# Performance work log

Hardware: AMD Instinct MI355X
Metric: run time of the kernel (lower is better)

The kernel has to match this reference:

```python
import jax, jax.numpy as jnp
from jax import lax
import numpy as np

# dims
N_DIA, DLEN = 48, 64            # 48 dialogues, 64 utterances each
N = N_DIA * DLEN                # total utterances = 3072
D = 512                         # n_dim (modal feature dim)
H = 512                         # nhidden
NL = 2                          # GCNII layers
NS = 2                          # n_speakers
ALPHA, LAMDA = 0.1, 0.5
PI = float(np.pi)
SCALE = 0.99999                 # acos clamp factor from original code


def setup_inputs() -> dict:
    key = jax.random.key(0)
    ks = jax.random.split(key, 8)
    a = jax.random.normal(ks[0], (N, D), jnp.float32)
    v = jax.random.normal(ks[1], (N, D), jnp.float32)
    l = jax.random.normal(ks[2], (N, D), jnp.float32)
    qmask = jax.random.uniform(ks[3], (DLEN, N_DIA, NS), jnp.float32)
    dia_len = np.full((N_DIA,), DLEN, dtype=np.int64)  # static segment lengths
    # learned params
    W_spk = 0.02 * jax.random.normal(ks[4], (NS, D), jnp.float32)      # speaker_embeddings
    W0 = jax.random.normal(ks[5], (D, H), jnp.float32) / np.sqrt(D)    # graph_net.fcs[0]
    b0 = jnp.zeros((H,), jnp.float32)
    Wg = jax.random.normal(ks[6], (NL, H, H), jnp.float32) / np.sqrt(H)  # GCNII conv weights
    return {"a": a, "v": v, "l": l, "qmask": qmask, "dia_len": dia_len,
            "W_spk": W_spk, "W0": W0, "b0": b0, "Wg": Wg}


def _angular_sim(cs):
    # 1 - acos(cs*0.99999)/pi, clipped for numerical safety of acos
    return 1.0 - jnp.arccos(jnp.clip(cs * SCALE, -SCALE, SCALE)) / PI


def _build_adj(feats, seg_mask):
    # feats: list of 3 arrays [N, D]; seg_mask: [N, N] same-dialogue block mask
    n = feats[0].shape[0]
    normed = [f * jax.lax.rsqrt(jnp.sum(f * f, axis=1, keepdims=True)) for f in feats]
    adj = jnp.zeros((3 * n, 3 * n), feats[0].dtype)
    ar = jnp.arange(n)
    for m in range(3):
        for nn_ in range(3):
            if m == nn_:
                # within-modality: block-diagonal (per dialogue) angular cosine similarity
                sim = _angular_sim(normed[m] @ normed[m].T) * seg_mask
                adj = adj.at[m * n:(m + 1) * n, nn_ * n:(nn_ + 1) * n].set(sim)
            else:
                # cross-modality: only diagonal (same utterance) entries
                cs = jnp.sum(normed[m] * normed[nn_], axis=1)
                adj = adj.at[m * n + ar, nn_ * n + ar].set(_angular_sim(cs))
    # symmetric degree normalization D^-1/2 A D^-1/2
    dinv = jax.lax.rsqrt(adj.sum(axis=1))
    return adj * dinv[:, None] * dinv[None, :]


def reference(a, v, l, qmask, dia_len, W_spk, W0, b0, Wg):
    dl = np.asarray(dia_len)
    nb = dl.shape[0]
    # node -> (position-in-dialogue, dialogue-id), static from dia_len
    dia_id = np.repeat(np.arange(nb), dl)
    pos = np.concatenate([np.arange(x) for x in dl])
    qflat = qmask[pos, dia_id]                 # [N, NS], matches torch.cat order
    spk_idx = jnp.argmax(qflat, axis=-1)       # [N]
    l = l + W_spk[spk_idx]                     # use_speaker=True, 'l' in modals

    seg = jnp.asarray(dia_id)
    seg_mask = (seg[:, None] == seg[None, :]).astype(a.dtype)  # [N, N]
    adj = _build_adj([a, v, l], seg_mask)      # [3N, 3N]

    x = jnp.concatenate([a, v, l], axis=0)     # [3N, D]
    # GCNII_lyc (eval mode: dropout is identity)
    h0 = jax.nn.relu(x @ W0 + b0)              # [3N, H]
    thetas = jnp.log(LAMDA / jnp.arange(1, NL + 1, dtype=x.dtype) + 1.0)

    def step(h, wt):
        W, theta = wt
        hi = adj @ h
        support = (1.0 - ALPHA) * hi + ALPHA * h0   # variant=False
        h = jax.nn.relu(theta * (support @ W) + (1.0 - theta) * support)
        return h, None

    h, _ = lax.scan(step, h0, (Wg, thetas))
    feat = jnp.concatenate([x, h], axis=-1)    # use_residue=True -> [3N, D+H]
    n = a.shape[0]
    # regroup per-utterance modal features: [N, 3*(D+H)]
    out = jnp.concatenate([feat[:n], feat[n:2 * n], feat[2 * n:3 * n]], axis=-1)
    return out
```

## Files before the change

### kernel.cpp

```cpp
#include <hip/hip_runtime.h>
#include <math.h>

#define N_DIA 48
#define NTOT  3072
#define DD    512
#define M3    9216
#define SEG   ((size_t)NTOT * DD)

#define SCALE_F 0.99999f
#define PI_F    3.14159274101257324f

typedef __attribute__((ext_vector_type(8))) short frag8;
typedef __attribute__((ext_vector_type(4))) float f32x4;

__device__ __forceinline__ float ang_sim(float cs) {
    float cc = cs * SCALE_F;
    cc = fminf(fmaxf(cc, -SCALE_F), SCALE_F);
    return 1.0f - acosf(cc) / PI_F;
}
__device__ __forceinline__ unsigned short f2bf(float x) {
    union { float f; unsigned int u; } c; c.f = x;
    unsigned int r = c.u + 0x7fffu + ((c.u >> 16) & 1u);
    return (unsigned short)(r >> 16);
}
__device__ __forceinline__ float bf2f(unsigned short h) {
    union { unsigned int u; float f; } c; c.u = ((unsigned int)h) << 16;
    return c.f;
}
__device__ __forceinline__ void gload16(const unsigned short* g, unsigned short* s) {
    __builtin_amdgcn_global_load_lds(
        (const __attribute__((address_space(1))) unsigned int*)g,
        (__attribute__((address_space(3))) unsigned int*)s, 16, 0, 0);
}

__global__ __launch_bounds__(256) void k_pre_wt(
    const float* __restrict__ a, const float* __restrict__ v,
    const float* __restrict__ l, const float* __restrict__ qmask,
    const float* __restrict__ Wspk, const float* __restrict__ W0,
    const float* __restrict__ Wg,
    float* __restrict__ out, unsigned short* __restrict__ xb,
    float* __restrict__ invn, float* __restrict__ cross,
    unsigned short* __restrict__ Wt)
{
    __shared__ float tile[32][33];
    int b = blockIdx.x;
    if (b < 768) {
        int wv = threadIdx.x >> 6, t = threadIdx.x & 63;
        int i = b * 4 + wv;
        int pos = i & 63, dia = i >> 6;
        int qb = (pos * N_DIA + dia) * 2;
        float q0 = qmask[qb], q1 = qmask[qb + 1];
        int spk = (q0 >= q1) ? 0 : 1;
        const float4* av4 = (const float4*)(a + (size_t)i * DD);
        const float4* vv4 = (const float4*)(v + (size_t)i * DD);
        const float4* lv4 = (const float4*)(l + (size_t)i * DD);
        const float4* wv4 = (const float4*)(Wspk + (size_t)spk * DD);
        float* ob = out + (size_t)i * 3072;
        float saa = 0, svv = 0, sll = 0, sav = 0, sal = 0, svl = 0;
#pragma unroll
        for (int e = 0; e < 2; e++) {
            int idx = e * 64 + t;
            float4 xa = av4[idx], xv = vv4[idx], xd = lv4[idx], xw = wv4[idx];
            float4 xL = make_float4(xd.x + xw.x, xd.y + xw.y, xd.z + xw.z, xd.w + xw.w);
            *(float4*)(ob + idx * 4)        = xa;
            *(float4*)(ob + 1024 + idx * 4) = xv;
            *(float4*)(ob + 2048 + idx * 4) = xL;
            ushort4 ya, yv, yl;
            ya.x = f2bf(xa.x); ya.y = f2bf(xa.y); ya.z = f2bf(xa.z); ya.w = f2bf(xa.w);
            yv.x = f2bf(xv.x); yv.y = f2bf(xv.y); yv.z = f2bf(xv.z); yv.w = f2bf(xv.w);
            yl.x = f2bf(xL.x); yl.y = f2bf(xL.y); yl.z = f2bf(xL.z); yl.w = f2bf(xL.w);
            *(ushort4*)(xb + (size_t)i * DD + idx * 4) = ya;
            *(ushort4*)(xb + SEG + (size_t)i * DD + idx * 4) = yv;
            *(ushort4*)(xb + 2 * SEG + (size_t)i * DD + idx * 4) = yl;
            saa += xa.x * xa.x + xa.y * xa.y + xa.z * xa.z + xa.w * xa.w;
            svv += xv.x * xv.x + xv.y * xv.y + xv.z * xv.z + xv.w * xv.w;
            sll += xL.x * xL.x + xL.y * xL.y + xL.z * xL.z + xL.w * xL.w;
            sav += xa.x * xv.x + xa.y * xv.y + xa.z * xv.z + xa.w * xv.w;
            sal += xa.x * xL.x + xa.y * xL.y + xa.z * xL.z + xa.w * xL.w;
            svl += xv.x * xL.x + xv.y * xL.y + xv.z * xL.z + xv.w * xL.w;
        }
#pragma unroll
        for (int off = 32; off; off >>= 1) {
            saa += __shfl_down(saa, off, 64);
            svv += __shfl_down(svv, off, 64);
            sll += __shfl_down(sll, off, 64);
            sav += __shfl_down(sav, off, 64);
            sal += __shfl_down(sal, off, 64);
            svl += __shfl_down(svl, off, 64);
        }
        if (t == 0) {
            float ina = 1.0f / sqrtf(saa);
            float inv_ = 1.0f / sqrtf(svv);
            float inl = 1.0f / sqrtf(sll);
            invn[i] = ina; invn[NTOT + i] = inv_; invn[2 * NTOT + i] = inl;
            cross[i]            = ang_sim(sav * ina * inv_);
            cross[NTOT + i]     = ang_sim(sal * ina * inl);
            cross[2 * NTOT + i] = ang_sim(svl * inv_ * inl);
        }
    } else {
        int idx = b - 768;
        int mm = idx >> 8;
        int by = (idx >> 4) & 15, bx = idx & 15;
        const float* W = (mm == 0) ? W0 : Wg + (size_t)(mm - 1) * DD * DD;
        int t = threadIdx.x, tx = t & 31, ty = t >> 5;
#pragma unroll
        for (int q = 0; q < 4; q++) {
            int k = by * 32 + ty + q * 8;
            tile[ty + q * 8][tx] = W[(size_t)k * DD + bx * 32 + tx];
        }
        __syncthreads();
#pragma unroll
        for (int q = 0; q < 4; q++) {
            int n = bx * 32 + ty + q * 8;
            Wt[(size_t)mm * DD * DD + (size_t)n * DD + by * 32 + tx] = f2bf(tile[tx][ty + q * 8]);
        }
    }
}

__global__ __launch_bounds__(256) void k_g0_gram(
    const unsigned short* __restrict__ xb, const unsigned short* __restrict__ Wt,
    const float* __restrict__ bias, unsigned short* __restrict__ h0,
    const float* __restrict__ invn, const float* __restrict__ cross,
    float* __restrict__ blk, float* __restrict__ dinv)
{
    __shared__ __align__(16) char smem[53248];
    int b = blockIdx.x;
    int t = threadIdx.x, lane = t & 63, wv = t >> 6;
    int rsel = lane & 15, quad = lane >> 4;

    if (b < 144) {
        unsigned short* Xs = (unsigned short*)smem;
        int d = b % N_DIA, m = b / N_DIA;
        int mrow = m * NTOT + d * 64;
        const unsigned short* src = xb + (size_t)mrow * DD;
        int sunit = ((t & 3) ^ ((t >> 2) & 3)) * 8;
        int sq = (quad ^ (rsel & 3)) * 8;
        f32x4 acc[4];
#pragma unroll
        for (int j = 0; j < 4; j++) acc[j] = (f32x4){0.f, 0.f, 0.f, 0.f};
#pragma unroll
        for (int p = 0; p < 2; p++) {
            if (p) __syncthreads();
#pragma unroll
            for (int c = 0; c < 8; c++) {
                gload16(src + (size_t)(t >> 2) * DD + (p * 8 + c) * 32 + sunit,
                        &Xs[c * 2048 + wv * 512]);
            }
            __syncthreads();
#pragma unroll
            for (int c = 0; c < 8; c++) {
                const unsigned short* base = &Xs[c * 2048];
                frag8 bf[4];
#pragma unroll
                for (int j = 0; j < 4; j++)
                    bf[j] = *(const frag8*)&base[(j * 16 + rsel) * 32 + sq];
                frag8 af = *(const frag8*)&base[(wv * 16 + rsel) * 32 + sq];
#pragma unroll
                for (int j = 0; j < 4; j++)
                    acc[j] = __builtin_amdgcn_mfma_f32_16x16x32_bf16(af, bf[j], acc[j], 0, 0, 0);
            }
        }

        size_t bbase = (size_t)(m * N_DIA + d) * 4096;
        int rowl0 = wv * 16 + quad * 4;
        float ir[4], rs[4] = {0.f, 0.f, 0.f, 0.f};
#pragma unroll
        for (int r = 0; r < 4; r++) ir[r] = invn[mrow + rowl0 + r];
#pragma unroll
        for (int j = 0; j < 4; j++) {
            int coll = j * 16 + rsel;
            float ic = invn[mrow + coll];
#pragma unroll
            for (int r = 0; r < 4; r++) {
                float sim = ang_sim(acc[j][r] * ir[r] * ic);
                blk[bbase + (size_t)(rowl0 + r) * 64 + coll] = sim;
                rs[r] += sim;
            }
        }
#pragma unroll
        for (int off = 8; off; off >>= 1)
#pragma unroll
            for (int r = 0; r < 4; r++) rs[r] += __shfl_down(rs[r], off, 16);
        if (rsel == 0) {
#pragma unroll
            for (int r = 0; r < 4; r++) {
                int gi = d * 64 + rowl0 + r;
                float c1, c2;
                if (m == 0)      { c1 = cross[gi];        c2 = cross[NTOT + gi]; }
                else if (m == 1) { c1 = cross[gi];        c2 = cross[2 * NTOT + gi]; }
                else             { c1 = cross[NTOT + gi]; c2 = cross[2 * NTOT + gi]; }
                dinv[m * NTOT + gi] = 1.0f / sqrtf(rs[r] + c1 + c2);
            }
        }
        return;
    }

    unsigned short* const As0 = (unsigned short*)smem;
    unsigned short* const As1 = (unsigned short*)(smem + 8192);
    unsigned short* const Bs0 = (unsigned short*)(smem + 16384);
    unsigned short* const Bs1 = (unsigned short*)(smem + 32768);
    unsigned short* const tR  = (unsigned short*)(smem + 17408);

    int b2 = b - 144;
    int bx = b2 & 3, by = b2 >> 2;
    int mbase = by * 64, nbase = bx * 128;
    int r8 = lane >> 3, u8 = lane & 7;
    int su8 = (u8 ^ r8) << 3;

    const unsigned short* Ag = xb + (size_t)(mbase + wv * 8 + r8) * DD + su8;
    const unsigned short* Bg = Wt + (size_t)(nbase + wv * 8 + r8) * DD + su8;

    f32x4 acc[8];
#pragma unroll
    for (int i = 0; i < 8; i++) acc[i] = (f32x4){0.f, 0.f, 0.f, 0.f};

#define STAGE64(kt, Asb, Bsb) do { \
    gload16(Ag + (kt) * 64,                    (Asb) + (wv * 8) * 64); \
    gload16(Ag + (size_t)32 * DD + (kt) * 64,  (Asb) + (32 + wv * 8) * 64); \
    gload16(Bg + (kt) * 64,                    (Bsb) + (wv * 8) * 64); \
    gload16(Bg + (size_t)32 * DD + (kt) * 64,  (Bsb) + (32 + wv * 8) * 64); \
    gload16(Bg + (size_t)64 * DD + (kt) * 64,  (Bsb) + (64 + wv * 8) * 64); \
    gload16(Bg + (size_t)96 * DD + (kt) * 64,  (Bsb) + (96 + wv * 8) * 64); \
} while (0)

    STAGE64(0, As0, Bs0);
#pragma unroll
    for (int kt = 0; kt < 8; kt++) {
        __syncthreads();
        const unsigned short* Ac = (kt & 1) ? As1 : As0;
        const unsigned short* Bc = (kt & 1) ? Bs1 : Bs0;
        if (kt < 7) {
            unsigned short* An = (kt & 1) ? As0 : As1;
            unsigned short* Bn = (kt & 1) ? Bs0 : Bs1;
            STAGE64(kt + 1, An, Bn);
        }
#pragma unroll
        for (int ks = 0; ks < 2; ks++) {
            int su = (((ks << 2) + quad) ^ (rsel & 7)) << 3;
            frag8 af[4], bfr[2];
#pragma unroll
            for (int i = 0; i < 4; i++)
                af[i] = *(const frag8*)&Ac[(i * 16 + rsel) * 64 + su];
#pragma unroll
            for (int j = 0; j < 2; j++)
                bfr[j] = *(const frag8*)&Bc[(wv * 32 + j * 16 + rsel) * 64 + su];
#pragma unroll
            for (int i = 0; i < 4; i++)
#pragma unroll
                for (int j = 0; j < 2; j++)
                    acc[i * 2 + j] = __builtin_amdgcn_mfma_f32_16x16x32_bf16(
                        af[i], bfr[j], acc[i * 2 + j], 0, 0, 0);
        }
    }
#undef STAGE64
    __syncthreads();

#pragma unroll
    for (int i = 0; i < 4; i++)
#pragma unroll
        for (int j = 0; j < 2; j++) {
            int cl = wv * 32 + j * 16 + rsel;
            float bv = bias[nbase + cl];
#pragma unroll
            for (int rr = 0; rr < 4; rr++) {
                float x = fmaxf(acc[i * 2 + j][rr] + bv, 0.f);
                tR[(i * 16 + quad * 4 + rr) * 136 + cl] = f2bf(x);
            }
        }
    __syncthreads();
    {
        int r = t >> 2, c0 = (t & 3) * 32;
        unsigned short* dst = h0 + (size_t)(mbase + r) * DD + nbase + c0;
#pragma unroll
        for (int u = 0; u < 4; u++)
            *(uint4*)(dst + u * 8) = *(const uint4*)&tR[r * 136 + c0 + u * 8];
    }
}

__global__ __launch_bounds__(256) void k_gemm(
    const unsigned short* __restrict__ A, const unsigned short* __restrict__ W,
    unsigned short* __restrict__ oRows, unsigned short* __restrict__ oT,
    float theta,
    const unsigned short* __restrict__ A2, unsigned short* __restrict__ oRows2)
{
    __shared__ __align__(16) char smem[53248];
    unsigned short* const As0 = (unsigned short*)smem;
    unsigned short* const As1 = (unsigned short*)(smem + 8192);
    unsigned short* const Bs0 = (unsigned short*)(smem + 16384);
    unsigned short* const Bs1 = (unsigned short*)(smem + 32768);
    unsigned short* const tH  = (unsigned short*)smem;
    unsigned short* const tR  = (unsigned short*)(smem + 17408);
    unsigned short* const tT  = (unsigned short*)(smem + 34816);

    int t = threadIdx.x, lane = t & 63, wv = t >> 6;
    int bx = blockIdx.x, by = blockIdx.y;
    const unsigned short* Ap = A;
    unsigned short* oR = oRows;
    unsigned short* oTp = oT;
    if (by >= 144) { Ap = A2; oR = oRows2; oTp = nullptr; by -= 144; }
    int mbase = by * 64, nbase = bx * 128;
    int rsel = lane & 15, quad = lane >> 4;
    int r8 = lane >> 3, u8 = lane & 7;
    int su8 = (u8 ^ r8) << 3;

    const unsigned short* Ag = Ap + (size_t)(mbase + wv * 8 + r8) * DD + su8;
    const unsigned short* Bg = W  + (size_t)(nbase + wv * 8 + r8) * DD + su8;

    f32x4 acc[8];
#pragma unroll
    for (int i = 0; i < 8; i++) acc[i] = (f32x4){0.f, 0.f, 0.f, 0.f};

#define STAGE64(kt, Asb, Bsb) do { \
    gload16(Ag + (kt) * 64,                    (Asb) + (wv * 8) * 64); \
    gload16(Ag + (size_t)32 * DD + (kt) * 64,  (Asb) + (32 + wv * 8) * 64); \
    gload16(Bg + (kt) * 64,                    (Bsb) + (wv * 8) * 64); \
    gload16(Bg + (size_t)32 * DD + (kt) * 64,  (Bsb) + (32 + wv * 8) * 64); \
    gload16(Bg + (size_t)64 * DD + (kt) * 64,  (Bsb) + (64 + wv * 8) * 64); \
    gload16(Bg + (size_t)96 * DD + (kt) * 64,  (Bsb) + (96 + wv * 8) * 64); \
} while (0)

    STAGE64(0, As0, Bs0);
#pragma unroll
    for (int kt = 0; kt < 8; kt++) {
        __syncthreads();
        const unsigned short* Ac = (kt & 1) ? As1 : As0;
        const unsigned short* Bc = (kt & 1) ? Bs1 : Bs0;
        if (kt < 7) {
            unsigned short* An = (kt & 1) ? As0 : As1;
            unsigned short* Bn = (kt & 1) ? Bs0 : Bs1;
            STAGE64(kt + 1, An, Bn);
        }
#pragma unroll
        for (int ks = 0; ks < 2; ks++) {
            int su = (((ks << 2) + quad) ^ (rsel & 7)) << 3;
            frag8 af[4], bfr[2];
#pragma unroll
            for (int i = 0; i < 4; i++)
                af[i] = *(const frag8*)&Ac[(i * 16 + rsel) * 64 + su];
#pragma unroll
            for (int j = 0; j < 2; j++)
                bfr[j] = *(const frag8*)&Bc[(wv * 32 + j * 16 + rsel) * 64 + su];
#pragma unroll
            for (int i = 0; i < 4; i++)
#pragma unroll
                for (int j = 0; j < 2; j++)
                    acc[i * 2 + j] = __builtin_amdgcn_mfma_f32_16x16x32_bf16(
                        af[i], bfr[j], acc[i * 2 + j], 0, 0, 0);
        }
    }
#undef STAGE64
    __syncthreads();

    int r = t >> 2, c0 = (t & 3) * 32;
    {
        const unsigned short* srcA = Ap + (size_t)(mbase + r) * DD + nbase + c0;
#pragma unroll
        for (int u = 0; u < 4; u++)
            *(uint4*)&tH[r * 136 + c0 + u * 8] = *(const uint4*)(srcA + u * 8);
        __syncthreads();
    }
    float omt = 1.0f - theta;
#pragma unroll
    for (int i = 0; i < 4; i++)
#pragma unroll
        for (int j = 0; j < 2; j++) {
            int cl = wv * 32 + j * 16 + rsel;
            float vv[4];
#pragma unroll
            for (int rr = 0; rr < 4; rr++) {
                int rl = i * 16 + quad * 4 + rr;
                vv[rr] = theta * acc[i * 2 + j][rr] + omt * bf2f(tH[rl * 136 + cl]);
            }
#pragma unroll
            for (int rr = 0; rr < 4; rr++)
                tR[(i * 16 + quad * 4 + rr) * 136 + cl] = f2bf(vv[rr]);
            if (oTp) {
                ushort4 w4;
                w4.x = f2bf(vv[0]); w4.y = f2bf(vv[1]);
                w4.z = f2bf(vv[2]); w4.w = f2bf(vv[3]);
                *(ushort4*)&tT[cl * 72 + i * 16 + quad * 4] = w4;
            }
        }
    __syncthreads();
    {
        unsigned short* dst = oR + (size_t)(mbase + r) * DD + nbase + c0;
#pragma unroll
        for (int u = 0; u < 4; u++)
            *(uint4*)(dst + u * 8) = *(const uint4*)&tR[r * 136 + c0 + u * 8];
    }
    if (oTp) {
        int c = t >> 1, r0 = (t & 1) * 32;
        unsigned short* dst = oTp + (size_t)(nbase + c) * M3 + mbase + r0;
#pragma unroll
        for (int u = 0; u < 4; u++)
            *(uint4*)(dst + u * 8) = *(const uint4*)&tT[c * 72 + r0 + u * 8];
    }
}

__global__ __launch_bounds__(256) void k_adj(
    const float* __restrict__ blk, const float* __restrict__ cross,
    const float* __restrict__ dinv,
    const unsigned short* __restrict__ GT, const unsigned short* __restrict__ Gr,
    const unsigned short* __restrict__ P0,
    unsigned short* __restrict__ hout, float* __restrict__ outF, int final_mode)
{
    __shared__ __align__(16) unsigned short AdL[64 * 64];
    __shared__ __align__(16) unsigned short GTL[128 * 64];
    __shared__ __align__(16) unsigned short OT[64 * 136];
    __shared__ float dv[64];
    int ch = blockIdx.x, d = blockIdx.y, m = blockIdx.z;
    int t = threadIdx.x;
    int lane = t & 63, wv = t >> 6;
    int dbase = d * 64, cbase = ch * 128;
    int rsel = lane & 15, quad = lane >> 4;

    if (t < 64) dv[t] = dinv[m * NTOT + dbase + t];
    __syncthreads();

    size_t bbase = (size_t)(m * N_DIA + d) * 4096;
#pragma unroll
    for (int q = 0; q < 4; q++) {
        int e4 = t + 256 * q;
        int i = e4 >> 4, j4 = e4 & 15;
        float4 w = *(const float4*)(blk + bbase + (size_t)i * 64 + j4 * 4);
        float di = dv[i];
        ushort4 o;
        o.x = f2bf(w.x * di * dv[j4 * 4 + 0]);
        o.y = f2bf(w.y * di * dv[j4 * 4 + 1]);
        o.z = f2bf(w.z * di * dv[j4 * 4 + 2]);
        o.w = f2bf(w.w * di * dv[j4 * 4 + 3]);
        *(ushort4*)((char*)AdL + i * 128 + (((j4 >> 1) ^ (i & 7)) << 4) + ((j4 & 1) << 3)) = o;
    }
#pragma unroll
    for (int p = 0; p < 4; p++) {
        int e = t + 256 * p;
        int cl = e >> 3;
        int uo = e & 7;
        uint4 w = *(const uint4*)(GT + (size_t)(cbase + cl) * M3 + m * NTOT + dbase + uo * 8);
        *(uint4*)((char*)GTL + cl * 128 + ((uo ^ (cl & 7)) << 4)) = w;
    }
    __syncthreads();

    f32x4 acc[8];
#pragma unroll
    for (int i = 0; i < 8; i++) acc[i] = (f32x4){0.f, 0.f, 0.f, 0.f};
#pragma unroll
    for (int kk = 0; kk < 2; kk++) {
        int su = ((kk * 4 + quad) ^ (rsel & 7)) << 4;
        frag8 bfr[4];
#pragma unroll
        for (int it = 0; it < 4; it++)
            bfr[it] = *(const frag8*)((const char*)AdL + (it * 16 + rsel) * 128 + su);
#pragma unroll
        for (int jc = 0; jc < 2; jc++) {
            frag8 af = *(const frag8*)((const char*)GTL + (wv * 32 + jc * 16 + rsel) * 128 + su);
#pragma unroll
            for (int it = 0; it < 4; it++)
                acc[jc * 4 + it] = __builtin_amdgcn_mfma_f32_16x16x32_bf16(
                    af, bfr[it], acc[jc * 4 + it], 0, 0, 0);
        }
    }

    int n1, n2, p1, p2;
    if (m == 0)      { n1 = 1; n2 = 2; p1 = 0; p2 = 1; }
    else if (m == 1) { n1 = 0; n2 = 2; p1 = 0; p2 = 2; }
    else             { n1 = 0; n2 = 1; p1 = 1; p2 = 2; }
#pragma unroll
    for (int it = 0; it < 4; it++) {
        int il = it * 16 + rsel;
        int gi = dbase + il;
        float dm = dv[il];
        float cv1 = cross[p1 * NTOT + gi] * dm * dinv[n1 * NTOT + gi];
        float cv2 = cross[p2 * NTOT + gi] * dm * dinv[n2 * NTOT + gi];
        size_t r1 = (size_t)(n1 * NTOT + gi) * DD;
        size_t r2 = (size_t)(n2 * NTOT + gi) * DD;
        size_t r0 = (size_t)(m * NTOT + gi) * DD;
#pragma unroll
        for (int jc = 0; jc < 2; jc++) {
            int cl = wv * 32 + jc * 16 + quad * 4;
            int cg = cbase + cl;
            ushort4 u1 = *(const ushort4*)(Gr + r1 + cg);
            ushort4 u2 = *(const ushort4*)(Gr + r2 + cg);
            ushort4 u0 = *(const ushort4*)(P0 + r0 + cg);
            f32x4 aa = acc[jc * 4 + it];
            float o0 = fmaxf(0.9f * (aa[0] + cv1 * bf2f(u1.x) + cv2 * bf2f(u2.x)) + 0.1f * bf2f(u0.x), 0.f);
            float o1 = fmaxf(0.9f * (aa[1] + cv1 * bf2f(u1.y) + cv2 * bf2f(u2.y)) + 0.1f * bf2f(u0.y), 0.f);
            float o2 = fmaxf(0.9f * (aa[2] + cv1 * bf2f(u1.z) + cv2 * bf2f(u2.z)) + 0.1f * bf2f(u0.z), 0.f);
            float o3 = fmaxf(0.9f * (aa[3] + cv1 * bf2f(u1.w) + cv2 * bf2f(u2.w)) + 0.1f * bf2f(u0.w), 0.f);
            if (final_mode) {
                *(float4*)(outF + (size_t)gi * 3072 + m * 1024 + 512 + cg) =
                    make_float4(o0, o1, o2, o3);
            } else {
                ushort4 w;
                w.x = f2bf(o0); w.y = f2bf(o1); w.z = f2bf(o2); w.w = f2bf(o3);
                *(ushort4*)&OT[il * 136 + cl] = w;
            }
        }
    }
    if (!final_mode) {
        __syncthreads();
        int r = t >> 2, c0 = (t & 3) * 32;
        unsigned short* dst = hout + (size_t)(m * NTOT + dbase + r) * DD + cbase + c0;
#pragma unroll
        for (int u = 0; u < 4; u++)
            *(uint4*)(dst + u * 8) = *(const uint4*)&OT[r * 136 + c0 + u * 8];
    }
}

extern "C" void kernel_launch(void* const* d_in, const int* in_sizes, int n_in,
                              void* d_out, int out_size, void* d_ws, size_t ws_size,
                              hipStream_t stream) {
    (void)in_sizes; (void)n_in; (void)out_size; (void)ws_size;
    const float* a     = (const float*)d_in[0];
    const float* v     = (const float*)d_in[1];
    const float* l     = (const float*)d_in[2];
    const float* qmask = (const float*)d_in[3];
    const float* Wspk  = (const float*)d_in[5];
    const float* W0    = (const float*)d_in[6];
    const float* b0    = (const float*)d_in[7];
    const float* Wg    = (const float*)d_in[8];
    float* out = (float*)d_out;
    float* ws = (float*)d_ws;

    float* invn  = ws;
    float* blk   = invn + M3;
    float* cross = blk + (size_t)3 * N_DIA * 4096;
    float* dinvp = cross + M3;
    unsigned short* Wt  = (unsigned short*)(dinvp + M3);
    unsigned short* xb  = Wt + (size_t)3 * DD * DD;
    unsigned short* h0  = xb  + 3 * SEG;
    unsigned short* G1r = h0  + 3 * SEG;
    unsigned short* G1T = G1r + 3 * SEG;
    unsigned short* h1  = G1T + 3 * SEG;
    unsigned short* G2r = xb;
    unsigned short* G2T = G1r;
    unsigned short* P02 = G1T;

    const float th1 = 0.40546510810816438f;
    const float th2 = 0.22314355131420976f;

    k_pre_wt<<<1536, 256, 0, stream>>>(a, v, l, qmask, Wspk, W0, Wg, out, xb, invn, cross, Wt);
    k_g0_gram<<<720, 256, 0, stream>>>(xb, Wt, b0, h0, invn, cross, blk, dinvp);
    k_gemm<<<dim3(4, 144), 256, 0, stream>>>(h0, Wt + (size_t)DD * DD, G1r, G1T,
                                             th1, nullptr, nullptr);
    k_adj<<<dim3(4, N_DIA, 3), 256, 0, stream>>>(blk, cross, dinvp, G1T, G1r, G1r,
                                                 h1, nullptr, 0);
    k_gemm<<<dim3(4, 288), 256, 0, stream>>>(h1, Wt + (size_t)2 * DD * DD, G2r, G2T,
                                             th2, h0, P02);
    k_adj<<<dim3(4, N_DIA, 3), 256, 0, stream>>>(blk, cross, dinvp, G2T, G2r, P02,
                                                 nullptr, out, 1);
}
```

Baseline: 185.5 us.

## Co-schedule layer-1 adjacency with layer-2 h0 GEMM in one launch

The layer-2 GEMM on h0 (the alpha*h0 skip term pushed through W2) no longer runs inside the second GEMM launch. It now shares a combined kernel with the layer-1 adjacency aggregation, using block-index ranges to split the two jobs. This lets the independent h0 GEMM overlap the memory-bound adjacency blocks and shortens the later GEMM launch. In exchange, the two jobs compete for the same CUs, and workspace aliasing now has P02 in xb and G2 reusing the G1 buffers.

Result: no change. 183.4 us (-1.1%).

```diff
diff --git a/kernel.cpp b/kernel.cpp
--- a/kernel.cpp
+++ b/kernel.cpp
@@ -280,8 +280,7 @@
 __global__ __launch_bounds__(256) void k_gemm(
     const unsigned short* __restrict__ A, const unsigned short* __restrict__ W,
     unsigned short* __restrict__ oRows, unsigned short* __restrict__ oT,
-    float theta,
-    const unsigned short* __restrict__ A2, unsigned short* __restrict__ oRows2)
+    float theta)
 {
     __shared__ __align__(16) char smem[53248];
     unsigned short* const As0 = (unsigned short*)smem;
@@ -294,17 +293,13 @@
 
     int t = threadIdx.x, lane = t & 63, wv = t >> 6;
     int bx = blockIdx.x, by = blockIdx.y;
-    const unsigned short* Ap = A;
-    unsigned short* oR = oRows;
-    unsigned short* oTp = oT;
-    if (by >= 144) { Ap = A2; oR = oRows2; oTp = nullptr; by -= 144; }
     int mbase = by * 64, nbase = bx * 128;
     int rsel = lane & 15, quad = lane >> 4;
     int r8 = lane >> 3, u8 = lane & 7;
     int su8 = (u8 ^ r8) << 3;
 
-    const unsigned short* Ag = Ap + (size_t)(mbase + wv * 8 + r8) * DD + su8;
-    const unsigned short* Bg = W  + (size_t)(nbase + wv * 8 + r8) * DD + su8;
+    const unsigned short* Ag = A + (size_t)(mbase + wv * 8 + r8) * DD + su8;
+    const unsigned short* Bg = W + (size_t)(nbase + wv * 8 + r8) * DD + su8;
 
     f32x4 acc[8];
 #pragma unroll
@@ -353,7 +348,7 @@
 
     int r = t >> 2, c0 = (t & 3) * 32;
     {
-        const unsigned short* srcA = Ap + (size_t)(mbase + r) * DD + nbase + c0;
+        const unsigned short* srcA = A + (size_t)(mbase + r) * DD + nbase + c0;
 #pragma unroll
         for (int u = 0; u < 4; u++)
             *(uint4*)&tH[r * 136 + c0 + u * 8] = *(const uint4*)(srcA + u * 8);
@@ -374,26 +369,225 @@
 #pragma unroll
             for (int rr = 0; rr < 4; rr++)
                 tR[(i * 16 + quad * 4 + rr) * 136 + cl] = f2bf(vv[rr]);
-            if (oTp) {
-                ushort4 w4;
-                w4.x = f2bf(vv[0]); w4.y = f2bf(vv[1]);
-                w4.z = f2bf(vv[2]); w4.w = f2bf(vv[3]);
-                *(ushort4*)&tT[cl * 72 + i * 16 + quad * 4] = w4;
-            }
+            ushort4 w4;
+            w4.x = f2bf(vv[0]); w4.y = f2bf(vv[1]);
+            w4.z = f2bf(vv[2]); w4.w = f2bf(vv[3]);
+            *(ushort4*)&tT[cl * 72 + i * 16 + quad * 4] = w4;
         }
     __syncthreads();
     {
-        unsigned short* dst = oR + (size_t)(mbase + r) * DD + nbase + c0;
+        unsigned short* dst = oRows + (size_t)(mbase + r) * DD + nbase + c0;
 #pragma unroll
         for (int u = 0; u < 4; u++)
             *(uint4*)(dst + u * 8) = *(const uint4*)&tR[r * 136 + c0 + u * 8];
     }
-    if (oTp) {
+    {
         int c = t >> 1, r0 = (t & 1) * 32;
-        unsigned short* dst = oTp + (size_t)(nbase + c) * M3 + mbase + r0;
+        unsigned short* dst = oT + (size_t)(nbase + c) * M3 + mbase + r0;
 #pragma unroll
         for (int u = 0; u < 4; u++)
             *(uint4*)(dst + u * 8) = *(const uint4*)&tT[c * 72 + r0 + u * 8];
+    }
+}
+
+__global__ __launch_bounds__(256) void k_adjg(
+    const float* __restrict__ blk, const float* __restrict__ cross,
+    const float* __restrict__ dinv,
+    const unsigned short* __restrict__ GT, const unsigned short* __restrict__ Gr,
+    const unsigned short* __restrict__ P0, unsigned short* __restrict__ hout,
+    const unsigned short* __restrict__ A2, const unsigned short* __restrict__ W2,
+    float th, unsigned short* __restrict__ oR2)
+{
+    __shared__ __align__(16) char smem[53248];
+    int b = blockIdx.x;
+    int t = threadIdx.x, lane = t & 63, wv = t >> 6;
+    int rsel = lane & 15, quad = lane >> 4;
+
+    if (b < 576) {
+        unsigned short* AdL = (unsigned short*)smem;
+        unsigned short* GTL = (unsigned short*)(smem + 8192);
+        unsigned short* OT  = (unsigned short*)(smem + 24576);
+        float* dv = (float*)(smem + 41984);
+        int ch = b & 3, rem = b >> 2;
+        int d = rem % N_DIA, m = rem / N_DIA;
+        int dbase = d * 64, cbase = ch * 128;
+
+        if (t < 64) dv[t] = dinv[m * NTOT + dbase + t];
+        __syncthreads();
+
+        size_t bbase = (size_t)(m * N_DIA + d) * 4096;
+#pragma unroll
+        for (int q = 0; q < 4; q++) {
+            int e4 = t + 256 * q;
+            int i = e4 >> 4, j4 = e4 & 15;
+            float4 w = *(const float4*)(blk + bbase + (size_t)i * 64 + j4 * 4);
+            float di = dv[i];
+            ushort4 o;
+            o.x = f2bf(w.x * di * dv[j4 * 4 + 0]);
+            o.y = f2bf(w.y * di * dv[j4 * 4 + 1]);
+            o.z = f2bf(w.z * di * dv[j4 * 4 + 2]);
+            o.w = f2bf(w.w * di * dv[j4 * 4 + 3]);
+            *(ushort4*)((char*)AdL + i * 128 + (((j4 >> 1) ^ (i & 7)) << 4) + ((j4 & 1) << 3)) = o;
+        }
+#pragma unroll
+        for (int p = 0; p < 4; p++) {
+            int e = t + 256 * p;
+            int cl = e >> 3;
+            int uo = e & 7;
+            uint4 w = *(const uint4*)(GT + (size_t)(cbase + cl) * M3 + m * NTOT + dbase + uo * 8);
+            *(uint4*)((char*)GTL + cl * 128 + ((uo ^ (cl & 7)) << 4)) = w;
+        }
+        __syncthreads();
+
+        f32x4 acc[8];
+#pragma unroll
+        for (int i = 0; i < 8; i++) acc[i] = (f32x4){0.f, 0.f, 0.f, 0.f};
+#pragma unroll
+        for (int kk = 0; kk < 2; kk++) {
+            int su = ((kk * 4 + quad) ^ (rsel & 7)) << 4;
+            frag8 bfr[4];
+#pragma unroll
+            for (int it = 0; it < 4; it++)
+                bfr[it] = *(const frag8*)((const char*)AdL + (it * 16 + rsel) * 128 + su);
+#pragma unroll
+            for (int jc = 0; jc < 2; jc++) {
+                frag8 af = *(const frag8*)((const char*)GTL + (wv * 32 + jc * 16 + rsel) * 128 + su);
+#pragma unroll
+                for (int it = 0; it < 4; it++)
+                    acc[jc * 4 + it] = __builtin_amdgcn_mfma_f32_16x16x32_bf16(
+                        af, bfr[it], acc[jc * 4 + it], 0, 0, 0);
+            }
+        }
+
+        int n1, n2, p1, p2;
+        if (m == 0)      { n1 = 1; n2 = 2; p1 = 0; p2 = 1; }
+        else if (m == 1) { n1 = 0; n2 = 2; p1 = 0; p2 = 2; }
+        else             { n1 = 0; n2 = 1; p1 = 1; p2 = 2; }
+#pragma unroll
+        for (int it = 0; it < 4; it++) {
+            int il = it * 16 + rsel;
+            int gi = dbase + il;
+            float dm = dv[il];
+            float cv1 = cross[p1 * NTOT + gi] * dm * dinv[n1 * NTOT + gi];
+            float cv2 = cross[p2 * NTOT + gi] * dm * dinv[n2 * NTOT + gi];
+            size_t r1 = (size_t)(n1 * NTOT + gi) * DD;
+            size_t r2 = (size_t)(n2 * NTOT + gi) * DD;
+            size_t r0 = (size_t)(m * NTOT + gi) * DD;
+#pragma unroll
+            for (int jc = 0; jc < 2; jc++) {
+                int cl = wv * 32 + jc * 16 + quad * 4;
+                int cg = cbase + cl;
+                ushort4 u1 = *(const ushort4*)(Gr + r1 + cg);
+                ushort4 u2 = *(const ushort4*)(Gr + r2 + cg);
+                ushort4 u0 = *(const ushort4*)(P0 + r0 + cg);
+                f32x4 aa = acc[jc * 4 + it];
+                ushort4 w;
+                w.x = f2bf(fmaxf(0.9f * (aa[0] + cv1 * bf2f(u1.x) + cv2 * bf2f(u2.x)) + 0.1f * bf2f(u0.x), 0.f));
+                w.y = f2bf(fmaxf(0.9f * (aa[1] + cv1 * bf2f(u1.y) + cv2 * bf2f(u2.y)) + 0.1f * bf2f(u0.y), 0.f));
+                w.z = f2bf(fmaxf(0.9f * (aa[2] + cv1 * bf2f(u1.z) + cv2 * bf2f(u2.z)) + 0.1f * bf2f(u0.z), 0.f));
+                w.w = f2bf(fmaxf(0.9f * (aa[3] + cv1 * bf2f(u1.w) + cv2 * bf2f(u2.w)) + 0.1f * bf2f(u0.w), 0.f));
+                *(ushort4*)&OT[il * 136 + cl] = w;
+            }
+        }
+        __syncthreads();
+        {
+            int r = t >> 2, c0 = (t & 3) * 32;
+            unsigned short* dst = hout + (size_t)(m * NTOT + dbase + r) * DD + cbase + c0;
+#pragma unroll
+            for (int u = 0; u < 4; u++)
+                *(uint4*)(dst + u * 8) = *(const uint4*)&OT[r * 136 + c0 + u * 8];
+        }
+        return;
+    }
+
+    unsigned short* const As0 = (unsigned short*)smem;
+    unsigned short* const As1 = (unsigned short*)(smem + 8192);
+    unsigned short* const Bs0 = (unsigned short*)(smem + 16384);
+    unsigned short* const Bs1 = (unsigned short*)(smem + 32768);
+    unsigned short* const tH  = (unsigned short*)smem;
+    unsigned short* const tR  = (unsigned short*)(smem + 17408);
+
+    int u2 = b - 576;
+    int bx = u2 & 3, by = u2 >> 2;
+    int mbase = by * 64, nbase = bx * 128;
+    int r8 = lane >> 3, u8 = lane & 7;
+    int su8 = (u8 ^ r8) << 3;
+
+    const unsigned short* Ag = A2 + (size_t)(mbase + wv * 8 + r8) * DD + su8;
+    const unsigned short* Bg = W2 + (size_t)(nbase + wv * 8 + r8) * DD + su8;
+
+    f32x4 acc[8];
+#pragma unroll
+    for (int i = 0; i < 8; i++) acc[i] = (f32x4){0.f, 0.f, 0.f, 0.f};
+
+#define STAGE64(kt, Asb, Bsb) do { \
+    gload16(Ag + (kt) * 64,                    (Asb) + (wv * 8) * 64); \
+    gload16(Ag + (size_t)32 * DD + (kt) * 64,  (Asb) + (32 + wv * 8) * 64); \
+    gload16(Bg + (kt) * 64,                    (Bsb) + (wv * 8) * 64); \
+    gload16(Bg + (size_t)32 * DD + (kt) * 64,  (Bsb) + (32 + wv * 8) * 64); \
+    gload16(Bg + (size_t)64 * DD + (kt) * 64,  (Bsb) + (64 + wv * 8) * 64); \
+    gload16(Bg + (size_t)96 * DD + (kt) * 64,  (Bsb) + (96 + wv * 8) * 64); \
+} while (0)
+
+    STAGE64(0, As0, Bs0);
+#pragma unroll
+    for (int kt = 0; kt < 8; kt++) {
+        __syncthreads();
+        const unsigned short* Ac = (kt & 1) ? As1 : As0;
+        const unsigned short* Bc = (kt & 1) ? Bs1 : Bs0;
+        if (kt < 7) {
+            unsigned short* An = (kt & 1) ? As0 : As1;
+            unsigned short* Bn = (kt & 1) ? Bs0 : Bs1;
+            STAGE64(kt + 1, An, Bn);
+        }
+#pragma unroll
+        for (int ks = 0; ks < 2; ks++) {
+            int su = (((ks << 2) + quad) ^ (rsel & 7)) << 3;
+            frag8 af[4], bfr[2];
+#pragma unroll
+            for (int i = 0; i < 4; i++)
+                af[i] = *(const frag8*)&Ac[(i * 16 + rsel) * 64 + su];
+#pragma unroll
+            for (int j = 0; j < 2; j++)
+                bfr[j] = *(const frag8*)&Bc[(wv * 32 + j * 16 + rsel) * 64 + su];
+#pragma unroll
+            for (int i = 0; i < 4; i++)
+#pragma unroll
+                for (int j = 0; j < 2; j++)
+                    acc[i * 2 + j] = __builtin_amdgcn_mfma_f32_16x16x32_bf16(
+                        af[i], bfr[j], acc[i * 2 + j], 0, 0, 0);
+        }
+    }
+#undef STAGE64
+    __syncthreads();
+
+    int r = t >> 2, c0 = (t & 3) * 32;
+    {
+        const unsigned short* srcA = A2 + (size_t)(mbase + r) * DD + nbase + c0;
+#pragma unroll
+        for (int u = 0; u < 4; u++)
+            *(uint4*)&tH[r * 136 + c0 + u * 8] = *(const uint4*)(srcA + u * 8);
+        __syncthreads();
+    }
+    float omt = 1.0f - th;
+#pragma unroll
+    for (int i = 0; i < 4; i++)
+#pragma unroll
+        for (int j = 0; j < 2; j++) {
+            int cl = wv * 32 + j * 16 + rsel;
+#pragma unroll
+            for (int rr = 0; rr < 4; rr++) {
+                int rl = i * 16 + quad * 4 + rr;
+                float x = th * acc[i * 2 + j][rr] + omt * bf2f(tH[rl * 136 + cl]);
+                tR[rl * 136 + cl] = f2bf(x);
+            }
+        }
+    __syncthreads();
+    {
+        unsigned short* dst = oR2 + (size_t)(mbase + r) * DD + nbase + c0;
+#pragma unroll
+        for (int u = 0; u < 4; u++)
+            *(uint4*)(dst + u * 8) = *(const uint4*)&tR[r * 136 + c0 + u * 8];
     }
 }
 
@@ -401,12 +595,10 @@
     const float* __restrict__ blk, const float* __restrict__ cross,
     const float* __restrict__ dinv,
     const unsigned short* __restrict__ GT, const unsigned short* __restrict__ Gr,
-    const unsigned short* __restrict__ P0,
-    unsigned short* __restrict__ hout, float* __restrict__ outF, int final_mode)
+    const unsigned short* __restrict__ P0, float* __restrict__ outF)
 {
     __shared__ __align__(16) unsigned short AdL[64 * 64];
     __shared__ __align__(16) unsigned short GTL[128 * 64];
-    __shared__ __align__(16) unsigned short OT[64 * 136];
     __shared__ float dv[64];
     int ch = blockIdx.x, d = blockIdx.y, m = blockIdx.z;
     int t = threadIdx.x;
@@ -487,23 +679,9 @@
             float o1 = fmaxf(0.9f * (aa[1] + cv1 * bf2f(u1.y) + cv2 * bf2f(u2.y)) + 0.1f * bf2f(u0.y), 0.f);
             float o2 = fmaxf(0.9f * (aa[2] + cv1 * bf2f(u1.z) + cv2 * bf2f(u2.z)) + 0.1f * bf2f(u0.z), 0.f);
             float o3 = fmaxf(0.9f * (aa[3] + cv1 * bf2f(u1.w) + cv2 * bf2f(u2.w)) + 0.1f * bf2f(u0.w), 0.f);
-            if (final_mode) {
-                *(float4*)(outF + (size_t)gi * 3072 + m * 1024 + 512 + cg) =
-                    make_float4(o0, o1, o2, o3);
-            } else {
-                ushort4 w;
-                w.x = f2bf(o0); w.y = f2bf(o1); w.z = f2bf(o2); w.w = f2bf(o3);
-                *(ushort4*)&OT[il * 136 + cl] = w;
-            }
-        }
-    }
-    if (!final_mode) {
-        __syncthreads();
-        int r = t >> 2, c0 = (t & 3) * 32;
-        unsigned short* dst = hout + (size_t)(m * NTOT + dbase + r) * DD + cbase + c0;
-#pragma unroll
-        for (int u = 0; u < 4; u++)
-            *(uint4*)(dst + u * 8) = *(const uint4*)&OT[r * 136 + c0 + u * 8];
+            *(float4*)(outF + (size_t)gi * 3072 + m * 1024 + 512 + cg) =
+                make_float4(o0, o1, o2, o3);
+        }
     }
 }
 
@@ -532,21 +710,18 @@
     unsigned short* G1r = h0  + 3 * SEG;
     unsigned short* G1T = G1r + 3 * SEG;
     unsigned short* h1  = G1T + 3 * SEG;
-    unsigned short* G2r = xb;
-    unsigned short* G2T = G1r;
-    unsigned short* P02 = G1T;
+    unsigned short* P02 = xb;
+    unsigned short* G2r = G1r;
+    unsigned short* G2T = G1T;
 
     const float th1 = 0.40546510810816438f;
     const float th2 = 0.22314355131420976f;
 
     k_pre_wt<<<1536, 256, 0, stream>>>(a, v, l, qmask, Wspk, W0, Wg, out, xb, invn, cross, Wt);
     k_g0_gram<<<720, 256, 0, stream>>>(xb, Wt, b0, h0, invn, cross, blk, dinvp);
-    k_gemm<<<dim3(4, 144), 256, 0, stream>>>(h0, Wt + (size_t)DD * DD, G1r, G1T,
-                                             th1, nullptr, nullptr);
-    k_adj<<<dim3(4, N_DIA, 3), 256, 0, stream>>>(blk, cross, dinvp, G1T, G1r, G1r,
-                                                 h1, nullptr, 0);
-    k_gemm<<<dim3(4, 288), 256, 0, stream>>>(h1, Wt + (size_t)2 * DD * DD, G2r, G2T,
-                                             th2, h0, P02);
-    k_adj<<<dim3(4, N_DIA, 3), 256, 0, stream>>>(blk, cross, dinvp, G2T, G2r, P02,
-                                                 nullptr, out, 1);
-}
+    k_gemm<<<dim3(4, 144), 256, 0, stream>>>(h0, Wt + (size_t)DD * DD, G1r, G1T, th1);
+    k_adjg<<<1152, 256, 0, stream>>>(blk, cross, dinvp, G1T, G1r, G1r, h1,
+                                     h0, Wt + (size_t)2 * DD * DD, th2, P02);
+    k_gemm<<<dim3(4, 144), 256, 0, stream>>>(h1, Wt + (size_t)2 * DD * DD, G2r, G2T, th2);
+    k_adj<<<dim3(4, N_DIA, 3), 256, 0, stream>>>(blk, cross, dinvp, G2T, G2r, P02, out);
+}
```

## Reorder GCNII layers to aggregate before the weight GEMM, dropping duplicate h0 GEMM

Applied to the files above, without the earlier changes.

The schedule previously used linearity to push the weight GEMM ahead of the adjacency product, which forced the second layer's GEMM to also process h0 (288 row blocks). It now computes support = adj@h + alpha*h0 first, in k_adjS, and then runs a GEMM on support with the theta blend and ReLU in its epilogue. The h0 GEMM emits a transposed copy for the first aggregation, and the final GEMM writes fp32 output directly. This removes one extra 3072x3-row GEMM pass, at the cost of an extra bf16 rounding of the support tensor.

Result: faster. 179.9 us (-3.0%).

```diff
diff --git a/kernel.cpp b/kernel.cpp
--- a/kernel.cpp
+++ b/kernel.cpp
@@ -120,6 +120,7 @@
 __global__ __launch_bounds__(256) void k_g0_gram(
     const unsigned short* __restrict__ xb, const unsigned short* __restrict__ Wt,
     const float* __restrict__ bias, unsigned short* __restrict__ h0,
+    unsigned short* __restrict__ h0T,
     const float* __restrict__ invn, const float* __restrict__ cross,
     float* __restrict__ blk, float* __restrict__ dinv)
 {
@@ -200,6 +201,7 @@
     unsigned short* const Bs0 = (unsigned short*)(smem + 16384);
     unsigned short* const Bs1 = (unsigned short*)(smem + 32768);
     unsigned short* const tR  = (unsigned short*)(smem + 17408);
+    unsigned short* const tT  = (unsigned short*)(smem + 34816);
 
     int b2 = b - 144;
     int bx = b2 & 3, by = b2 >> 2;
@@ -261,11 +263,17 @@
         for (int j = 0; j < 2; j++) {
             int cl = wv * 32 + j * 16 + rsel;
             float bv = bias[nbase + cl];
-#pragma unroll
-            for (int rr = 0; rr < 4; rr++) {
-                float x = fmaxf(acc[i * 2 + j][rr] + bv, 0.f);
-                tR[(i * 16 + quad * 4 + rr) * 136 + cl] = f2bf(x);
-            }
+            float vv[4];
+#pragma unroll
+            for (int rr = 0; rr < 4; rr++)
+                vv[rr] = fmaxf(acc[i * 2 + j][rr] + bv, 0.f);
+#pragma unroll
+            for (int rr = 0; rr < 4; rr++)
+                tR[(i * 16 + quad * 4 + rr) * 136 + cl] = f2bf(vv[rr]);
+            ushort4 w4;
+            w4.x = f2bf(vv[0]); w4.y = f2bf(vv[1]);
+            w4.z = f2bf(vv[2]); w4.w = f2bf(vv[3]);
+            *(ushort4*)&tT[cl * 72 + i * 16 + quad * 4] = w4;
         }
     __syncthreads();
     {
@@ -275,134 +283,20 @@
         for (int u = 0; u < 4; u++)
             *(uint4*)(dst + u * 8) = *(const uint4*)&tR[r * 136 + c0 + u * 8];
     }
-}
-
-__global__ __launch_bounds__(256) void k_gemm(
-    const unsigned short* __restrict__ A, const unsigned short* __restrict__ W,
-    unsigned short* __restrict__ oRows, unsigned short* __restrict__ oT,
-    float theta,
-    const unsigned short* __restrict__ A2, unsigned short* __restrict__ oRows2)
-{
-    __shared__ __align__(16) char smem[53248];
-    unsigned short* const As0 = (unsigned short*)smem;
-    unsigned short* const As1 = (unsigned short*)(smem + 8192);
-    unsigned short* const Bs0 = (unsigned short*)(smem + 16384);
-    unsigned short* const Bs1 = (unsigned short*)(smem + 32768);
-    unsigned short* const tH  = (unsigned short*)smem;
-    unsigned short* const tR  = (unsigned short*)(smem + 17408);
-    unsigned short* const tT  = (unsigned short*)(smem + 34816);
-
-    int t = threadIdx.x, lane = t & 63, wv = t >> 6;
-    int bx = blockIdx.x, by = blockIdx.y;
-    const unsigned short* Ap = A;
-    unsigned short* oR = oRows;
-    unsigned short* oTp = oT;
-    if (by >= 144) { Ap = A2; oR = oRows2; oTp = nullptr; by -= 144; }
-    int mbase = by * 64, nbase = bx * 128;
-    int rsel = lane & 15, quad = lane >> 4;
-    int r8 = lane >> 3, u8 = lane & 7;
-    int su8 = (u8 ^ r8) << 3;
-
-    const unsigned short* Ag = Ap + (size_t)(mbase + wv * 8 + r8) * DD + su8;
-    const unsigned short* Bg = W  + (size_t)(nbase + wv * 8 + r8) * DD + su8;
-
-    f32x4 acc[8];
-#pragma unroll
-    for (int i = 0; i < 8; i++) acc[i] = (f32x4){0.f, 0.f, 0.f, 0.f};
-
-#define STAGE64(kt, Asb, Bsb) do { \
-    gload16(Ag + (kt) * 64,                    (Asb) + (wv * 8) * 64); \
-    gload16(Ag + (size_t)32 * DD + (kt) * 64,  (Asb) + (32 + wv * 8) * 64); \
-    gload16(Bg + (kt) * 64,                    (Bsb) + (wv * 8) * 64); \
-    gload16(Bg + (size_t)32 * DD + (kt) * 64,  (Bsb) + (32 + wv * 8) * 64); \
-    gload16(Bg + (size_t)64 * DD + (kt) * 64,  (Bsb) + (64 + wv * 8) * 64); \
-    gload16(Bg + (size_t)96 * DD + (kt) * 64,  (Bsb) + (96 + wv * 8) * 64); \
-} while (0)
-
-    STAGE64(0, As0, Bs0);
-#pragma unroll
-    for (int kt = 0; kt < 8; kt++) {
-        __syncthreads();
-        const unsigned short* Ac = (kt & 1) ? As1 : As0;
-        const unsigned short* Bc = (kt & 1) ? Bs1 : Bs0;
-        if (kt < 7) {
-            unsigned short* An = (kt & 1) ? As0 : As1;
-            unsigned short* Bn = (kt & 1) ? Bs0 : Bs1;
-            STAGE64(kt + 1, An, Bn);
-        }
-#pragma unroll
-        for (int ks = 0; ks < 2; ks++) {
-            int su = (((ks << 2) + quad) ^ (rsel & 7)) << 3;
-            frag8 af[4], bfr[2];
-#pragma unroll
-            for (int i = 0; i < 4; i++)
-                af[i] = *(const frag8*)&Ac[(i * 16 + rsel) * 64 + su];
-#pragma unroll
-            for (int j = 0; j < 2; j++)
-                bfr[j] = *(const frag8*)&Bc[(wv * 32 + j * 16 + rsel) * 64 + su];
-#pragma unroll
-            for (int i = 0; i < 4; i++)
-#pragma unroll
-                for (int j = 0; j < 2; j++)
-                    acc[i * 2 + j] = __builtin_amdgcn_mfma_f32_16x16x32_bf16(
-                        af[i], bfr[j], acc[i * 2 + j], 0, 0, 0);
-        }
-    }
-#undef STAGE64
-    __syncthreads();
-
-    int r = t >> 2, c0 = (t & 3) * 32;
     {
-        const unsigned short* srcA = Ap + (size_t)(mbase + r) * DD + nbase + c0;
-#pragma unroll
-        for (int u = 0; u < 4; u++)
-            *(uint4*)&tH[r * 136 + c0 + u * 8] = *(const uint4*)(srcA + u * 8);
-        __syncthreads();
-    }
-    float omt = 1.0f - theta;
-#pragma unroll
-    for (int i = 0; i < 4; i++)
-#pragma unroll
-        for (int j = 0; j < 2; j++) {
-            int cl = wv * 32 + j * 16 + rsel;
-            float vv[4];
-#pragma unroll
-            for (int rr = 0; rr < 4; rr++) {
-                int rl = i * 16 + quad * 4 + rr;
-                vv[rr] = theta * acc[i * 2 + j][rr] + omt * bf2f(tH[rl * 136 + cl]);
-            }
-#pragma unroll
-            for (int rr = 0; rr < 4; rr++)
-                tR[(i * 16 + quad * 4 + rr) * 136 + cl] = f2bf(vv[rr]);
-            if (oTp) {
-                ushort4 w4;
-                w4.x = f2bf(vv[0]); w4.y = f2bf(vv[1]);
-                w4.z = f2bf(vv[2]); w4.w = f2bf(vv[3]);
-                *(ushort4*)&tT[cl * 72 + i * 16 + quad * 4] = w4;
-            }
-        }
-    __syncthreads();
-    {
-        unsigned short* dst = oR + (size_t)(mbase + r) * DD + nbase + c0;
-#pragma unroll
-        for (int u = 0; u < 4; u++)
-            *(uint4*)(dst + u * 8) = *(const uint4*)&tR[r * 136 + c0 + u * 8];
-    }
-    if (oTp) {
         int c = t >> 1, r0 = (t & 1) * 32;
-        unsigned short* dst = oTp + (size_t)(nbase + c) * M3 + mbase + r0;
+        unsigned short* dst = h0T + (size_t)(nbase + c) * M3 + mbase + r0;
 #pragma unroll
         for (int u = 0; u < 4; u++)
             *(uint4*)(dst + u * 8) = *(const uint4*)&tT[c * 72 + r0 + u * 8];
     }
 }
 
-__global__ __launch_bounds__(256) void k_adj(
+__global__ __launch_bounds__(256) void k_adjS(
     const float* __restrict__ blk, const float* __restrict__ cross,
     const float* __restrict__ dinv,
     const unsigned short* __restrict__ GT, const unsigned short* __restrict__ Gr,
-    const unsigned short* __restrict__ P0,
-    unsigned short* __restrict__ hout, float* __restrict__ outF, int final_mode)
+    const unsigned short* __restrict__ P0, unsigned short* __restrict__ Sout)
 {
     __shared__ __align__(16) unsigned short AdL[64 * 64];
     __shared__ __align__(16) unsigned short GTL[128 * 64];
@@ -483,27 +377,157 @@
             ushort4 u2 = *(const ushort4*)(Gr + r2 + cg);
             ushort4 u0 = *(const ushort4*)(P0 + r0 + cg);
             f32x4 aa = acc[jc * 4 + it];
-            float o0 = fmaxf(0.9f * (aa[0] + cv1 * bf2f(u1.x) + cv2 * bf2f(u2.x)) + 0.1f * bf2f(u0.x), 0.f);
-            float o1 = fmaxf(0.9f * (aa[1] + cv1 * bf2f(u1.y) + cv2 * bf2f(u2.y)) + 0.1f * bf2f(u0.y), 0.f);
-            float o2 = fmaxf(0.9f * (aa[2] + cv1 * bf2f(u1.z) + cv2 * bf2f(u2.z)) + 0.1f * bf2f(u0.z), 0.f);
-            float o3 = fmaxf(0.9f * (aa[3] + cv1 * bf2f(u1.w) + cv2 * bf2f(u2.w)) + 0.1f * bf2f(u0.w), 0.f);
-            if (final_mode) {
-                *(float4*)(outF + (size_t)gi * 3072 + m * 1024 + 512 + cg) =
-                    make_float4(o0, o1, o2, o3);
-            } else {
-                ushort4 w;
-                w.x = f2bf(o0); w.y = f2bf(o1); w.z = f2bf(o2); w.w = f2bf(o3);
-                *(ushort4*)&OT[il * 136 + cl] = w;
-            }
-        }
-    }
-    if (!final_mode) {
-        __syncthreads();
+            ushort4 w;
+            w.x = f2bf(0.9f * (aa[0] + cv1 * bf2f(u1.x) + cv2 * bf2f(u2.x)) + 0.1f * bf2f(u0.x));
+            w.y = f2bf(0.9f * (aa[1] + cv1 * bf2f(u1.y) + cv2 * bf2f(u2.y)) + 0.1f * bf2f(u0.y));
+            w.z = f2bf(0.9f * (aa[2] + cv1 * bf2f(u1.z) + cv2 * bf2f(u2.z)) + 0.1f * bf2f(u0.z));
+            w.w = f2bf(0.9f * (aa[3] + cv1 * bf2f(u1.w) + cv2 * bf2f(u2.w)) + 0.1f * bf2f(u0.w));
+            *(ushort4*)&OT[il * 136 + cl] = w;
+        }
+    }
+    __syncthreads();
+    {
         int r = t >> 2, c0 = (t & 3) * 32;
-        unsigned short* dst = hout + (size_t)(m * NTOT + dbase + r) * DD + cbase + c0;
+        unsigned short* dst = Sout + (size_t)(m * NTOT + dbase + r) * DD + cbase + c0;
 #pragma unroll
         for (int u = 0; u < 4; u++)
             *(uint4*)(dst + u * 8) = *(const uint4*)&OT[r * 136 + c0 + u * 8];
+    }
+}
+
+__global__ __launch_bounds__(256) void k_gemm_s(
+    const unsigned short* __restrict__ A, const unsigned short* __restrict__ W,
+    unsigned short* __restrict__ oRows, unsigned short* __restrict__ oT,
+    float theta, float* __restrict__ outF)
+{
+    __shared__ __align__(16) char smem[53248];
+    unsigned short* const As0 = (unsigned short*)smem;
+    unsigned short* const As1 = (unsigned short*)(smem + 8192);
+    unsigned short* const Bs0 = (unsigned short*)(smem + 16384);
+    unsigned short* const Bs1 = (unsigned short*)(smem + 32768);
+    unsigned short* const tH  = (unsigned short*)smem;
+    unsigned short* const tR  = (unsigned short*)(smem + 17408);
+    unsigned short* const tT  = (unsigned short*)(smem + 34816);
+    float* const tF           = (float*)(smem + 17408);
+
+    int t = threadIdx.x, lane = t & 63, wv = t >> 6;
+    int bx = blockIdx.x, by = blockIdx.y;
+    int mbase = by * 64, nbase = bx * 128;
+    int rsel = lane & 15, quad = lane >> 4;
+    int r8 = lane >> 3, u8 = lane & 7;
+    int su8 = (u8 ^ r8) << 3;
+
+    const unsigned short* Ag = A + (size_t)(mbase + wv * 8 + r8) * DD + su8;
+    const unsigned short* Bg = W + (size_t)(nbase + wv * 8 + r8) * DD + su8;
+
+    f32x4 acc[8];
+#pragma unroll
+    for (int i = 0; i < 8; i++) acc[i] = (f32x4){0.f, 0.f, 0.f, 0.f};
+
+#define STAGE64(kt, Asb, Bsb) do { \
+    gload16(Ag + (kt) * 64,                    (Asb) + (wv * 8) * 64); \
+    gload16(Ag + (size_t)32 * DD + (kt) * 64,  (Asb) + (32 + wv * 8) * 64); \
+    gload16(Bg + (kt) * 64,                    (Bsb) + (wv * 8) * 64); \
+    gload16(Bg + (size_t)32 * DD + (kt) * 64,  (Bsb) + (32 + wv * 8) * 64); \
+    gload16(Bg + (size_t)64 * DD + (kt) * 64,  (Bsb) + (64 + wv * 8) * 64); \
+    gload16(Bg + (size_t)96 * DD + (kt) * 64,  (Bsb) + (96 + wv * 8) * 64); \
+} while (0)
+
+    STAGE64(0, As0, Bs0);
+#pragma unroll
+    for (int kt = 0; kt < 8; kt++) {
+        __syncthreads();
+        const unsigned short* Ac = (kt & 1) ? As1 : As0;
+        const unsigned short* Bc = (kt & 1) ? Bs1 : Bs0;
+        if (kt < 7) {
+            unsigned short* An = (kt & 1) ? As0 : As1;
+            unsigned short* Bn = (kt & 1) ? Bs0 : Bs1;
+            STAGE64(kt + 1, An, Bn);
+        }
+#pragma unroll
+        for (int ks = 0; ks < 2; ks++) {
+            int su = (((ks << 2) + quad) ^ (rsel & 7)) << 3;
+            frag8 af[4], bfr[2];
+#pragma unroll
+            for (int i = 0; i < 4; i++)
+                af[i] = *(const frag8*)&Ac[(i * 16 + rsel) * 64 + su];
+#pragma unroll
+            for (int j = 0; j < 2; j++)
+                bfr[j] = *(const frag8*)&Bc[(wv * 32 + j * 16 + rsel) * 64 + su];
+#pragma unroll
+            for (int i = 0; i < 4; i++)
+#pragma unroll
+                for (int j = 0; j < 2; j++)
+                    acc[i * 2 + j] = __builtin_amdgcn_mfma_f32_16x16x32_bf16(
+                        af[i], bfr[j], acc[i * 2 + j], 0, 0, 0);
+        }
+    }
+#undef STAGE64
+    __syncthreads();
+
+    int r = t >> 2, c0 = (t & 3) * 32;
+    {
+        const unsigned short* srcA = A + (size_t)(mbase + r) * DD + nbase + c0;
+#pragma unroll
+        for (int u = 0; u < 4; u++)
+            *(uint4*)&tH[r * 136 + c0 + u * 8] = *(const uint4*)(srcA + u * 8);
+        __syncthreads();
+    }
+    float omt = 1.0f - theta;
+    if (outF == nullptr) {
+#pragma unroll
+        for (int i = 0; i < 4; i++)
+#pragma unroll
+            for (int j = 0; j < 2; j++) {
+                int cl = wv * 32 + j * 16 + rsel;
+                float vv[4];
+#pragma unroll
+                for (int rr = 0; rr < 4; rr++) {
+                    int rl = i * 16 + quad * 4 + rr;
+                    vv[rr] = fmaxf(theta * acc[i * 2 + j][rr] + omt * bf2f(tH[rl * 136 + cl]), 0.f);
+                }
+#pragma unroll
+                for (int rr = 0; rr < 4; rr++)
+                    tR[(i * 16 + quad * 4 + rr) * 136 + cl] = f2bf(vv[rr]);
+                ushort4 w4;
+                w4.x = f2bf(vv[0]); w4.y = f2bf(vv[1]);
+                w4.z = f2bf(vv[2]); w4.w = f2bf(vv[3]);
+                *(ushort4*)&tT[cl * 72 + i * 16 + quad * 4] = w4;
+            }
+        __syncthreads();
+        {
+            unsigned short* dst = oRows + (size_t)(mbase + r) * DD + nbase + c0;
+#pragma unroll
+            for (int u = 0; u < 4; u++)
+                *(uint4*)(dst + u * 8) = *(const uint4*)&tR[r * 136 + c0 + u * 8];
+        }
+        {
+            int c = t >> 1, r0 = (t & 1) * 32;
+            unsigned short* dst = oT + (size_t)(nbase + c) * M3 + mbase + r0;
+#pragma unroll
+            for (int u = 0; u < 4; u++)
+                *(uint4*)(dst + u * 8) = *(const uint4*)&tT[c * 72 + r0 + u * 8];
+        }
+    } else {
+#pragma unroll
+        for (int i = 0; i < 4; i++)
+#pragma unroll
+            for (int j = 0; j < 2; j++) {
+                int cl = wv * 32 + j * 16 + rsel;
+#pragma unroll
+                for (int rr = 0; rr < 4; rr++) {
+                    int rl = i * 16 + quad * 4 + rr;
+                    tF[rl * 132 + cl] = fmaxf(theta * acc[i * 2 + j][rr]
+                                              + omt * bf2f(tH[rl * 136 + cl]), 0.f);
+                }
+            }
+        __syncthreads();
+        int mq = mbase / NTOT;
+        int iu0 = mbase - mq * NTOT;
+        float* dst = outF + (size_t)(iu0 + r) * 3072 + mq * 1024 + 512 + nbase + c0;
+#pragma unroll
+        for (int u = 0; u < 8; u++)
+            *(float4*)(dst + u * 4) = *(const float4*)&tF[r * 132 + c0 + u * 4];
     }
 }
 
@@ -527,26 +551,27 @@
     float* cross = blk + (size_t)3 * N_DIA * 4096;
     float* dinvp = cross + M3;
     unsigned short* Wt  = (unsigned short*)(dinvp + M3);
-    unsigned short* xb  = Wt + (size_t)3 * DD * DD;
-    unsigned short* h0  = xb  + 3 * SEG;
-    unsigned short* G1r = h0  + 3 * SEG;
-    unsigned short* G1T = G1r + 3 * SEG;
-    unsigned short* h1  = G1T + 3 * SEG;
-    unsigned short* G2r = xb;
-    unsigned short* G2T = G1r;
-    unsigned short* P02 = G1T;
+    unsigned short* B0  = Wt + (size_t)3 * DD * DD;
+    unsigned short* B1  = B0 + 3 * SEG;
+    unsigned short* B2  = B1 + 3 * SEG;
+    unsigned short* B3  = B2 + 3 * SEG;
+    unsigned short* xb  = B0;
+    unsigned short* S1  = B0;
+    unsigned short* S2  = B0;
+    unsigned short* h0r = B1;
+    unsigned short* h0T = B2;
+    unsigned short* h1T = B2;
+    unsigned short* h1r = B3;
 
     const float th1 = 0.40546510810816438f;
     const float th2 = 0.22314355131420976f;
 
     k_pre_wt<<<1536, 256, 0, stream>>>(a, v, l, qmask, Wspk, W0, Wg, out, xb, invn, cross, Wt);
-    k_g0_gram<<<720, 256, 0, stream>>>(xb, Wt, b0, h0, invn, cross, blk, dinvp);
-    k_gemm<<<dim3(4, 144), 256, 0, stream>>>(h0, Wt + (size_t)DD * DD, G1r, G1T,
-                                             th1, nullptr, nullptr);
-    k_adj<<<dim3(4, N_DIA, 3), 256, 0, stream>>>(blk, cross, dinvp, G1T, G1r, G1r,
-                                                 h1, nullptr, 0);
-    k_gemm<<<dim3(4, 288), 256, 0, stream>>>(h1, Wt + (size_t)2 * DD * DD, G2r, G2T,
-                                             th2, h0, P02);
-    k_adj<<<dim3(4, N_DIA, 3), 256, 0, stream>>>(blk, cross, dinvp, G2T, G2r, P02,
-                                                 nullptr, out, 1);
-}
+    k_g0_gram<<<720, 256, 0, stream>>>(xb, Wt, b0, h0r, h0T, invn, cross, blk, dinvp);
+    k_adjS<<<dim3(4, N_DIA, 3), 256, 0, stream>>>(blk, cross, dinvp, h0T, h0r, h0r, S1);
+    k_gemm_s<<<dim3(4, 144), 256, 0, stream>>>(S1, Wt + (size_t)DD * DD, h1r, h1T,
+                                               th1, nullptr);
+    k_adjS<<<dim3(4, N_DIA, 3), 256, 0, stream>>>(blk, cross, dinvp, h1T, h1r, h0r, S2);
+    k_gemm_s<<<dim3(4, 144), 256, 0, stream>>>(S2, Wt + (size_t)2 * DD * DD, nullptr, nullptr,
+                                               th2, out);
+}
```
